# Performance work log

Hardware: AMD Instinct MI355X
Metric: run time of the kernel (lower is better)

Reference implementation:

```python
import jax, jax.numpy as jnp
import numpy as np

NUM_LAYERS = 4
EPS = 1e-8


def setup_inputs() -> dict:
    key = jax.random.key(0)
    ks = jax.random.split(key, 7)
    N, D, H = 8192, 1024, 4096
    return {
        "x": jax.random.normal(ks[0], (N, D), jnp.float32),
        "fc1_W": jax.random.normal(ks[1], (H, D), jnp.float32) * 0.02,
        "fc1_b": jax.random.normal(ks[2], (H,), jnp.float32) * 0.02,
        "fc2_W": jax.random.normal(ks[3], (D, H), jnp.float32) * 0.02,
        "fc2_b": jax.random.normal(ks[4], (D,), jnp.float32) * 0.02,
        "comp_W": jax.random.normal(ks[5], (NUM_LAYERS + 1, D, D), jnp.float32) * 0.03,
        "comp_b": jax.random.normal(ks[6], (NUM_LAYERS + 1, D), jnp.float32) * 0.03,
    }


def _block(x, fc1_W, fc1_b, fc2_W, fc2_b):
    # fc2(dropout(fc1(x))) in eval mode; relu is defined but never applied
    h = x @ fc1_W.T + fc1_b
    return h @ fc2_W.T + fc2_b


def _compute_loss(z, W, b):
    # out = Linear(z); per-row cosine_similarity(out_i.unsqueeze(1), out_i.unsqueeze(0))
    # reduces broadcast dim 1 -> vector c[j] = out[j]*sum(out) / max(|out[j]|*sqrt(y)*||out||, eps)
    # which torch broadcasts into constant rows of a [y,y] matrix; the
    # abs-diff accumulation over batch rows is then rank-1.
    out = z @ W.T + b                                # [N, y]
    y = out.shape[-1]
    S = out.sum(-1, keepdims=True)                   # [N, 1]
    n2 = jnp.sqrt((out * out).sum(-1, keepdims=True))  # [N, 1] row norms
    n1 = jnp.abs(out) * jnp.sqrt(jnp.asarray(y, out.dtype))  # [N, y]
    c = out * S / jnp.maximum(n1 * n2, EPS)          # [N, y]
    D = jnp.abs(c[1:] - c[:-1]).sum(0)               # [y]
    return jnp.broadcast_to(D, (y, y))               # [y, y]


def reference(x, fc1_W, fc1_b, fc2_W, fc2_b, comp_W, comp_b):
    inv = _block(x, fc1_W, fc1_b, fc2_W, fc2_b)
    loss = _compute_loss(inv, comp_W[0], comp_b[0])
    nxt = x - inv
    inv_total = inv
    for i in range(1, NUM_LAYERS + 1):
        inv_new = _block(nxt, fc1_W, fc1_b, fc2_W, fc2_b)
        inv_total = inv_total + inv_new
        loss = loss + _compute_loss(inv_new, comp_W[i], comp_b[i])
        nxt = nxt - inv_new
    return inv_total, nxt, loss
```

## Files before the change

kernel.cpp:

```cpp
#include <hip/hip_runtime.h>
#include <hip/hip_bf16.h>


#define NR 8192
#define DD 1024
#define HH 4096
#define NL 5
#define MSZ (DD * DD)

using bf16 = __hip_bfloat16;
typedef __attribute__((ext_vector_type(8))) short bf16x8;
typedef __attribute__((ext_vector_type(4))) float f32x4;
typedef _Float16 h4 __attribute__((ext_vector_type(4)));


__global__ void cvt_bf16_kernel(const float* __restrict__ in, bf16* __restrict__ out, int n4) {
  int i = blockIdx.x * 256 + threadIdx.x;
  int stride = gridDim.x * 256;
  union U { bf16 b[4]; uint2 u; };
  for (; i < n4; i += stride) {
    float4 v = ((const float4*)in)[i];
    U u;
    u.b[0] = __float2bfloat16(v.x); u.b[1] = __float2bfloat16(v.y);
    u.b[2] = __float2bfloat16(v.z); u.b[3] = __float2bfloat16(v.w);
    ((uint2*)out)[i] = u.u;
  }
}

__global__ void transpose_cvt_kernel(const float* __restrict__ in, bf16* __restrict__ out) {
  __shared__ bf16 tile[64][74];
  int c0 = blockIdx.x * 64;
  int r0 = blockIdx.y * 64;
  int col = threadIdx.x & 63;
  int row4 = threadIdx.x >> 6;
  #pragma unroll
  for (int j = 0; j < 16; ++j) {
    int r = row4 * 16 + j;
    tile[r][col] = __float2bfloat16(in[(size_t)(r0 + r) * DD + c0 + col]);
  }
  __syncthreads();
  #pragma unroll
  for (int j = 0; j < 16; ++j) {
    int r = row4 * 16 + j;
    out[(size_t)(c0 + r) * HH + r0 + col] = tile[col][r];
  }
}

__global__ void cvec_kernel(const float* __restrict__ fc1_b, const float* __restrict__ fc2_W,
                            const float* __restrict__ fc2_b, float* __restrict__ c) {
  int j = blockIdx.x;
  float s = 0.f;
  for (int k = threadIdx.x; k < HH; k += 256) s += fc1_b[k] * fc2_W[(size_t)j * HH + k];
  for (int o = 32; o; o >>= 1) s += __shfl_down(s, o);
  __shared__ float red[4];
  if ((threadIdx.x & 63) == 0) red[threadIdx.x >> 6] = s;
  __syncthreads();
  if (threadIdx.x == 0) c[j] = red[0] + red[1] + red[2] + red[3] + fc2_b[j];
}

__global__ void zero_kernel(float* __restrict__ p, int n) {
  int i = blockIdx.x * 256 + threadIdx.x;
  if (i < n) p[i] = 0.f;
}

__global__ void mbuild_kernel(const float* __restrict__ Cp,
                              bf16* __restrict__ M, bf16* __restrict__ Mt,
                              bf16* __restrict__ T, bf16* __restrict__ Tt) {
  __shared__ float tile[64][65];
  int n0 = blockIdx.x * 64, m0 = blockIdx.y * 64;
  int tn = threadIdx.x & 63, tm4 = threadIdx.x >> 6;
  #pragma unroll
  for (int j = 0; j < 16; ++j) {
    int m = tm4 * 16 + j;
    size_t idx = (size_t)(m0 + m) * DD + n0 + tn;
    float v = Cp[idx] + Cp[MSZ + idx] + Cp[2 * MSZ + idx] + Cp[3 * MSZ + idx];
    tile[m][tn] = v;
    float d = ((m0 + m) == (n0 + tn)) ? 1.f : 0.f;
    M[idx] = __float2bfloat16(v);
    T[idx] = __float2bfloat16(d - v);
  }
  __syncthreads();
  #pragma unroll
  for (int j = 0; j < 16; ++j) {
    int r = tm4 * 16 + j;
    float v = tile[tn][r];
    size_t idx = (size_t)(n0 + r) * DD + m0 + tn;
    float d = ((n0 + r) == (m0 + tn)) ? 1.f : 0.f;
    Mt[idx] = __float2bfloat16(v);
    Tt[idx] = __float2bfloat16(d - v);
  }
}

__global__ void sbuild_kernel(const bf16* __restrict__ Pw, bf16* __restrict__ S) {
  int idx = blockIdx.x * 256 + threadIdx.x;
  int m = idx >> 10, n = idx & (DD - 1);
  float v = (m == n) ? 1.f : 0.f;
  v += __bfloat162float(Pw[idx]) + __bfloat162float(Pw[MSZ + idx])
     + __bfloat162float(Pw[2 * MSZ + idx]) + __bfloat162float(Pw[3 * MSZ + idx]);
  S[idx] = __float2bfloat16(v);
}

__global__ void vecmat_kernel(const float* __restrict__ v, const bf16* __restrict__ Bt,
                              float* __restrict__ out) {
  int z = blockIdx.y, j = blockIdx.x;
  const bf16* row = Bt + (size_t)z * MSZ + (size_t)j * DD;
  float s = 0.f;
  for (int k = threadIdx.x; k < DD; k += 256) s += v[k] * __bfloat162float(row[k]);
  for (int o = 32; o; o >>= 1) s += __shfl_down(s, o);
  __shared__ float red[4];
  if ((threadIdx.x & 63) == 0) red[threadIdx.x >> 6] = s;
  __syncthreads();
  if (threadIdx.x == 0) out[(size_t)z * DD + j] = red[0] + red[1] + red[2] + red[3];
}

__global__ void biasall_kernel(const float* __restrict__ cvec, const float* __restrict__ ebuf,
                               const float* __restrict__ comp_W, const float* __restrict__ comp_b,
                               float* __restrict__ biasall) {
  int z = blockIdx.y, j = blockIdx.x;
  if (z == 0) {
    if (threadIdx.x == 0)
      biasall[j] = cvec[j] + ebuf[j] + ebuf[DD + j] + ebuf[2 * DD + j] + ebuf[3 * DD + j];
    return;
  }
  int i = z - 1;
  const float* e = (i == 0) ? cvec : ebuf + (size_t)(i - 1) * DD;
  const float* wr = comp_W + (size_t)i * MSZ + (size_t)j * DD;
  float s = 0.f;
  for (int k = threadIdx.x; k < DD; k += 256) s += e[k] * wr[k];
  for (int o = 32; o; o >>= 1) s += __shfl_down(s, o);
  __shared__ float red[4];
  if ((threadIdx.x & 63) == 0) red[threadIdx.x >> 6] = s;
  __syncthreads();
  if (threadIdx.x == 0)
    biasall[(size_t)z * DD + j] = red[0] + red[1] + red[2] + red[3] + comp_b[(size_t)i * DD + j];
}


__device__ __forceinline__ void async16(const bf16* g, bf16* l) {
  __builtin_amdgcn_global_load_lds(
      (const __attribute__((address_space(1))) void*)g,
      (__attribute__((address_space(3))) void*)l, 16, 0, 0);
}

__device__ __forceinline__ void gemm_core_async(
    const bf16* __restrict__ A, const bf16* __restrict__ B,
    int kBeg, int kEnd, int lda, int ldb, int bm, int bn,
    bf16* As, bf16* Bs, f32x4 acc[4][4])
{
  const int tid  = threadIdx.x;
  const int lane = tid & 63;
  const int wave = tid >> 6;
  const int wm = (wave & 1) * 64;
  const int wn = (wave >> 1) * 64;
  const int lr = lane >> 3;
  const int lcol = ((lane & 7) ^ lr) * 8;
  const bf16* gA = A + (size_t)(bm + wave * 32 + lr) * lda + lcol;
  const bf16* gB = B + (size_t)(bn + wave * 32 + lr) * ldb + lcol;
  bf16* lA = As + wave * 32 * 64;
  bf16* lB = Bs + wave * 32 * 64;

  for (int k0 = kBeg; k0 < kEnd; k0 += 64) {
    #pragma unroll
    for (int it = 0; it < 4; ++it) {
      async16(gA + (size_t)(it * 8) * lda + k0, lA + it * 8 * 64);
      async16(gB + (size_t)(it * 8) * ldb + k0, lB + it * 8 * 64);
    }
    __syncthreads();
    #pragma unroll
    for (int ks = 0; ks < 2; ++ks) {
      bf16x8 av[4], bv[4];
      #pragma unroll
      for (int i = 0; i < 4; ++i) {
        const int rr = i * 16 + (lane & 15);
        const int cc = ((ks * 4 + (lane >> 4)) ^ (lane & 7)) * 8;
        av[i] = *(const bf16x8*)(As + (wm + rr) * 64 + cc);
        bv[i] = *(const bf16x8*)(Bs + (wn + rr) * 64 + cc);
      }
      #pragma unroll
      for (int i = 0; i < 4; ++i)
        #pragma unroll
        for (int j = 0; j < 4; ++j)
          acc[i][j] = __builtin_amdgcn_mfma_f32_16x16x32_bf16(av[i], bv[j], acc[i][j], 0, 0, 0);
    }
    __syncthreads();
  }
}

#define GEMM_PROLOGUE \
  alignas(16) __shared__ bf16 As[128 * 64]; \
  alignas(16) __shared__ bf16 Bs[128 * 64]; \
  f32x4 acc[4][4] = {}; \
  const int lane = threadIdx.x & 63; \
  const int wm = ((threadIdx.x >> 6) & 1) * 64; \
  const int wn = ((threadIdx.x >> 6) >> 1) * 64;

__global__ __launch_bounds__(256, 2)
void gemm_splitk(const bf16* __restrict__ A, const bf16* __restrict__ B, float* __restrict__ Cp) {
  GEMM_PROLOGUE
  const int bm = blockIdx.y * 128, bn = blockIdx.x * 128;
  const int kb = blockIdx.z * (HH / 4);
  gemm_core_async(A, B, kb, kb + HH / 4, HH, HH, bm, bn, As, Bs, acc);
  float* C = Cp + (size_t)blockIdx.z * MSZ;
  #pragma unroll
  for (int i = 0; i < 4; ++i)
    #pragma unroll
    for (int j = 0; j < 4; ++j) {
      const int col = bn + wn + j * 16 + (lane & 15);
      #pragma unroll
      for (int r = 0; r < 4; ++r) {
        const int row = bm + wm + i * 16 + (lane >> 4) * 4 + r;
        C[(size_t)row * DD + col] = acc[i][j][r];
      }
    }
}

__global__ __launch_bounds__(256, 2)
void gemm_dual(const bf16* __restrict__ A, const bf16* __restrict__ B,
               bf16* __restrict__ Ct, bf16* __restrict__ Cn) {
  GEMM_PROLOGUE
  const int bm = blockIdx.y * 128, bn = blockIdx.x * 128;
  gemm_core_async(A, B, 0, DD, DD, DD, bm, bn, As, Bs, acc);
  #pragma unroll
  for (int i = 0; i < 4; ++i)
    #pragma unroll
    for (int j = 0; j < 4; ++j) {
      const int col = bn + wn + j * 16 + (lane & 15);
      const int row0 = bm + wm + i * 16 + (lane >> 4) * 4;
      union { bf16 b[4]; uint2 u; } pk;
      #pragma unroll
      for (int r = 0; r < 4; ++r) {
        bf16 v = __float2bfloat16(acc[i][j][r]);
        pk.b[r] = v;
        Cn[(size_t)(row0 + r) * DD + col] = v;
      }
      *(uint2*)(&Ct[(size_t)col * DD + row0]) = pk.u;
    }
}

__global__ __launch_bounds__(256, 2)
void gemm_b4(const bf16* __restrict__ A0, long astr, const bf16* __restrict__ B0, long bstr,
             bf16* __restrict__ C0, long cstr,
             const bf16* __restrict__ A2, const bf16* __restrict__ B2, bf16* __restrict__ C2,
             int zswitch) {
  GEMM_PROLOGUE
  const int z = blockIdx.z;
  const bf16* A; const bf16* B; bf16* C;
  if (z < zswitch) { A = A0 + (size_t)z * astr; B = B0 + (size_t)z * bstr; C = C0 + (size_t)z * cstr; }
  else             { A = A2; B = B2; C = C2; }
  const int bm = blockIdx.y * 128, bn = blockIdx.x * 128;
  gemm_core_async(A, B, 0, DD, DD, DD, bm, bn, As, Bs, acc);
  #pragma unroll
  for (int i = 0; i < 4; ++i)
    #pragma unroll
    for (int j = 0; j < 4; ++j) {
      const int col = bn + wn + j * 16 + (lane & 15);
      #pragma unroll
      for (int r = 0; r < 4; ++r) {
        const int row = bm + wm + i * 16 + (lane >> 4) * 4 + r;
        C[(size_t)row * DD + col] = __float2bfloat16(acc[i][j][r]);
      }
    }
}

__global__ __launch_bounds__(256, 2)
void gemm_main(const bf16* __restrict__ A, const bf16* __restrict__ Bb,
               const float* __restrict__ biasall, const float* __restrict__ x,
               float* __restrict__ invtot, float* __restrict__ nxtf,
               _Float16* __restrict__ out_h, float* __restrict__ Srow, float* __restrict__ Qrow) {
  GEMM_PROLOGUE
  const int bm = blockIdx.y * 128, bn = blockIdx.x * 128;
  gemm_core_async(A, Bb + (size_t)(bn >> 10) * MSZ, 0, DD, DD, DD, bm, bn & (DD - 1), As, Bs, acc);

  if (bn < DD) {
    #pragma unroll
    for (int i = 0; i < 4; ++i)
      #pragma unroll
      for (int j = 0; j < 4; ++j) {
        const int col = bn + wn + j * 16 + (lane & 15);
        const float bj = biasall[col];
        #pragma unroll
        for (int r = 0; r < 4; ++r) {
          const int row = bm + wm + i * 16 + (lane >> 4) * 4 + r;
          const float v = acc[i][j][r] + bj;
          const size_t idx = (size_t)row * DD + col;
          invtot[idx] = v;
          nxtf[idx] = x[idx] - v;
        }
      }
  } else {
    const int z = (bn >> 10) - 1;
    _Float16* oz = out_h + (size_t)z * NR * DD;
    const int cbase = bn & (DD - 1);
    float sv[4][4] = {}, qv[4][4] = {};
    #pragma unroll
    for (int i = 0; i < 4; ++i)
      #pragma unroll
      for (int j = 0; j < 4; ++j) {
        const int colg = bn + wn + j * 16 + (lane & 15);
        const int cj = cbase + wn + j * 16 + (lane & 15);
        const float bj = biasall[colg];
        #pragma unroll
        for (int r = 0; r < 4; ++r) {
          const int row = bm + wm + i * 16 + (lane >> 4) * 4 + r;
          const float v = acc[i][j][r] + bj;
          oz[(size_t)row * DD + cj] = (_Float16)v;
          sv[i][r] += v;
          qv[i][r] += v * v;
        }
      }
    #pragma unroll
    for (int i = 0; i < 4; ++i)
      #pragma unroll
      for (int r = 0; r < 4; ++r) {
        float s = sv[i][r], q = qv[i][r];
        #pragma unroll
        for (int off = 1; off < 16; off <<= 1) { s += __shfl_xor(s, off); q += __shfl_xor(q, off); }
        if ((lane & 15) == 0) {
          const int row = bm + wm + i * 16 + (lane >> 4) * 4 + r;
          atomicAdd(&Srow[(size_t)z * NR + row], s);
          atomicAdd(&Qrow[(size_t)z * NR + row], q);
        }
      }
  }
}


#define LCR 64
__global__ void losscol2_kernel(const _Float16* __restrict__ oh, const float* __restrict__ Srow,
                                const float* __restrict__ Qrow, float* __restrict__ Dtot) {
  const int z = blockIdx.y;
  const int n0 = blockIdx.x * LCR;
  int nend = n0 + LCR; if (nend > NR - 1) nend = NR - 1;
  const _Float16* base = oh + (size_t)z * NR * DD + (size_t)threadIdx.x * 4;
  const float* S = Srow + (size_t)z * NR;
  const float* Q = Qrow + (size_t)z * NR;
  float c[4], d[4] = {0.f, 0.f, 0.f, 0.f};
  auto compute = [&](int n, float* cv) {
    h4 o = *(const h4*)(base + (size_t)n * DD);
    float s = S[n];
    float t = 32.0f * sqrtf(Q[n]);
    #pragma unroll
    for (int k = 0; k < 4; ++k) {
      float ov = (float)o[k];
      cv[k] = ov * s / fmaxf(fabsf(ov) * t, 1e-8f);
    }
  };
  compute(n0, c);
  for (int n = n0 + 1; n <= nend; ++n) {
    float cn[4];
    compute(n, cn);
    #pragma unroll
    for (int k = 0; k < 4; ++k) { d[k] += fabsf(cn[k] - c[k]); c[k] = cn[k]; }
  }
  #pragma unroll
  for (int k = 0; k < 4; ++k) atomicAdd(&Dtot[z * DD + threadIdx.x * 4 + k], d[k]);
}

__global__ void writeloss_kernel(const float* __restrict__ Dtot, float* __restrict__ out) {
  int idx = blockIdx.x * 256 + threadIdx.x;
  int j = idx & (DD - 1);
  out[idx] = Dtot[j] + Dtot[DD + j] + Dtot[2 * DD + j] + Dtot[3 * DD + j] + Dtot[4 * DD + j];
}


extern "C" void kernel_launch(void* const* d_in, const int* in_sizes, int n_in,
                              void* d_out, int out_size, void* d_ws, size_t ws_size,
                              hipStream_t stream) {
  const float* x      = (const float*)d_in[0];
  const float* fc1_W  = (const float*)d_in[1];
  const float* fc1_b  = (const float*)d_in[2];
  const float* fc2_W  = (const float*)d_in[3];
  const float* fc2_b  = (const float*)d_in[4];
  const float* comp_W = (const float*)d_in[5];
  const float* comp_b = (const float*)d_in[6];

  float* invtot  = (float*)d_out;
  float* nxtf    = invtot + (size_t)NR * DD;
  float* lossout = invtot + (size_t)2 * NR * DD;

  char* w = (char*)d_ws;
  auto alloc = [&](size_t bytes) { char* p = w; w += (bytes + 255) & ~(size_t)255; return p; };
  bf16* x_bf     = (bf16*)alloc((size_t)NR * DD * 2);
  bf16* fc1T_bf  = (bf16*)alloc((size_t)DD * HH * 2);
  bf16* fc2_bf   = (bf16*)alloc((size_t)DD * HH * 2);
  bf16* compW_bf = (bf16*)alloc((size_t)NL * MSZ * 2);
  bf16* M_bf     = (bf16*)alloc((size_t)MSZ * 2);
  bf16* Mt_bf    = (bf16*)alloc((size_t)MSZ * 2);
  bf16* Tt_buf   = (bf16*)alloc((size_t)2 * MSZ * 2);
  bf16* Pw       = (bf16*)alloc((size_t)4 * MSZ * 2);
  bf16* S_bf     = (bf16*)alloc((size_t)MSZ * 2);
  bf16* Gt       = (bf16*)alloc((size_t)NL * MSZ * 2);
  bf16* Bbig     = (bf16*)alloc((size_t)6 * MSZ * 2);
  _Float16* out_h = (_Float16*)alloc((size_t)NL * NR * DD * 2);
  float* cvec    = (float*)alloc(DD * 4);
  float* ebuf    = (float*)alloc((size_t)4 * DD * 4);
  float* biasall = (float*)alloc((size_t)6 * DD * 4);
  float* stats   = (float*)alloc((size_t)(NL * DD + 2 * NL * NR) * 4);
  float* Dtot = stats;
  float* Srow = stats + NL * DD;
  float* Qrow = Srow + (size_t)NL * NR;
  float* Cp = (float*)out_h;
  (void)ws_size; (void)in_sizes; (void)n_in; (void)out_size;

  cvt_bf16_kernel<<<2048, 256, 0, stream>>>(x, x_bf, NR * DD / 4);
  cvt_bf16_kernel<<<1024, 256, 0, stream>>>(fc2_W, fc2_bf, DD * HH / 4);
  cvt_bf16_kernel<<<1024, 256, 0, stream>>>(comp_W, compW_bf, NL * MSZ / 4);
  transpose_cvt_kernel<<<dim3(DD / 64, HH / 64), 256, 0, stream>>>(fc1_W, fc1T_bf);
  cvec_kernel<<<DD, 256, 0, stream>>>(fc1_b, fc2_W, fc2_b, cvec);
  zero_kernel<<<(NL * DD + 2 * NL * NR + 255) / 256, 256, 0, stream>>>(stats, NL * DD + 2 * NL * NR);

  gemm_splitk<<<dim3(8, 8, 4), 256, 0, stream>>>(fc1T_bf, fc2_bf, Cp);
  mbuild_kernel<<<dim3(16, 16), 256, 0, stream>>>(Cp, M_bf, Mt_bf, Pw, Tt_buf);
  gemm_b4<<<dim3(8, 8, NL), 256, 0, stream>>>(compW_bf, MSZ, M_bf, 0, Gt, MSZ,
                                              nullptr, nullptr, nullptr, 99);
  hipMemcpyAsync(Bbig + MSZ, Gt, (size_t)MSZ * 2, hipMemcpyDeviceToDevice, stream);
  gemm_dual<<<dim3(8, 8), 256, 0, stream>>>(Pw, Tt_buf, Tt_buf + MSZ, Pw + MSZ);
  gemm_b4<<<dim3(8, 8, 2), 256, 0, stream>>>(Pw + MSZ, 0, Tt_buf, MSZ, Pw + 2 * MSZ, MSZ,
                                             nullptr, nullptr, nullptr, 99);
  sbuild_kernel<<<MSZ / 256, 256, 0, stream>>>(Pw, S_bf);
  gemm_b4<<<dim3(8, 8, NL), 256, 0, stream>>>(Gt + MSZ, MSZ, Pw, MSZ, Bbig + 2 * MSZ, MSZ,
                                              Mt_bf, S_bf, Bbig, 4);
  vecmat_kernel<<<dim3(DD, 2), 256, 0, stream>>>(cvec, Tt_buf, ebuf);
  vecmat_kernel<<<dim3(DD, 2), 256, 0, stream>>>(ebuf + DD, Tt_buf, ebuf + 2 * DD);
  biasall_kernel<<<dim3(DD, 6), 256, 0, stream>>>(cvec, ebuf, comp_W, comp_b, biasall);

  gemm_main<<<dim3(6 * DD / 128, NR / 128), 256, 0, stream>>>(
      x_bf, Bbig, biasall, x, invtot, nxtf, out_h, Srow, Qrow);

  losscol2_kernel<<<dim3(NR / LCR, NL), 256, 0, stream>>>(out_h, Srow, Qrow, Dtot);
  writeloss_kernel<<<MSZ / 256, 256, 0, stream>>>(Dtot, lossout);
}
```

Before: 527.8 us.

## Store only output sign bits for loss instead of fp16 outputs

The loss term c = out*S/max(|out|*sqrt(y)*||out||, eps) reduces to sign(out)*S/(32*||out||), so the GEMM epilogue now records one sign bit per element via wave ballots instead of writing the full fp16 projected outputs. A new loss kernel rebuilds c from the sign bits and the per-row sum and norm, computing abs-diffs per column from a shared-memory table of row scales. This removes about 80MB of fp16 writes and reads. The exact-zero/eps edge case is treated differently, and the bit-packed layout makes the loss kernel's access pattern scattered.

```diff
diff --git a/kernel.cpp b/kernel.cpp
--- a/kernel.cpp
+++ b/kernel.cpp
@@ -11,7 +11,6 @@
 using bf16 = __hip_bfloat16;
 typedef __attribute__((ext_vector_type(8))) short bf16x8;
 typedef __attribute__((ext_vector_type(4))) float f32x4;
-typedef _Float16 h4 __attribute__((ext_vector_type(4)));
 
 
 __global__ void cvt_bf16_kernel(const float* __restrict__ in, bf16* __restrict__ out, int n4) {
@@ -266,7 +265,8 @@
 void gemm_main(const bf16* __restrict__ A, const bf16* __restrict__ Bb,
                const float* __restrict__ biasall, const float* __restrict__ x,
                float* __restrict__ invtot, float* __restrict__ nxtf,
-               _Float16* __restrict__ out_h, float* __restrict__ Srow, float* __restrict__ Qrow) {
+               unsigned long long* __restrict__ sgn,
+               float* __restrict__ Srow, float* __restrict__ Qrow) {
   GEMM_PROLOGUE
   const int bm = blockIdx.y * 128, bn = blockIdx.x * 128;
   gemm_core_async(A, Bb + (size_t)(bn >> 10) * MSZ, 0, DD, DD, DD, bm, bn & (DD - 1), As, Bs, acc);
@@ -289,25 +289,28 @@
       }
   } else {
     const int z = (bn >> 10) - 1;
-    _Float16* oz = out_h + (size_t)z * NR * DD;
-    const int cbase = bn & (DD - 1);
+    const int rb = bm >> 7;
+    const int cb = (bn & (DD - 1)) >> 7;
+    const int wave = threadIdx.x >> 6;
+    unsigned long long keep = 0ULL;
     float sv[4][4] = {}, qv[4][4] = {};
     #pragma unroll
     for (int i = 0; i < 4; ++i)
       #pragma unroll
       for (int j = 0; j < 4; ++j) {
         const int colg = bn + wn + j * 16 + (lane & 15);
-        const int cj = cbase + wn + j * 16 + (lane & 15);
         const float bj = biasall[colg];
         #pragma unroll
         for (int r = 0; r < 4; ++r) {
-          const int row = bm + wm + i * 16 + (lane >> 4) * 4 + r;
           const float v = acc[i][j][r] + bj;
-          oz[(size_t)row * DD + cj] = (_Float16)v;
+          const unsigned long long bal = __ballot(v < 0.f);
+          if (lane == i * 16 + j * 4 + r) keep = bal;
           sv[i][r] += v;
           qv[i][r] += v * v;
         }
       }
+    const size_t wbase = ((((size_t)z * 64 + rb) * 8 + cb) * 4 + wave) * 64;
+    sgn[wbase + lane] = keep;
     #pragma unroll
     for (int i = 0; i < 4; ++i)
       #pragma unroll
@@ -325,35 +328,50 @@
 }
 
 
-#define LCR 64
-__global__ void losscol2_kernel(const _Float16* __restrict__ oh, const float* __restrict__ Srow,
-                                const float* __restrict__ Qrow, float* __restrict__ Dtot) {
+__global__ void losssign_kernel(const unsigned long long* __restrict__ sgn,
+                                const float* __restrict__ Srow, const float* __restrict__ Qrow,
+                                float* __restrict__ Dtot) {
   const int z = blockIdx.y;
-  const int n0 = blockIdx.x * LCR;
-  int nend = n0 + LCR; if (nend > NR - 1) nend = NR - 1;
-  const _Float16* base = oh + (size_t)z * NR * DD + (size_t)threadIdx.x * 4;
+  const int cg = blockIdx.x;
+  const int n0 = blockIdx.z * 1024;
+  __shared__ float rsh[1025];
   const float* S = Srow + (size_t)z * NR;
   const float* Q = Qrow + (size_t)z * NR;
-  float c[4], d[4] = {0.f, 0.f, 0.f, 0.f};
-  auto compute = [&](int n, float* cv) {
-    h4 o = *(const h4*)(base + (size_t)n * DD);
-    float s = S[n];
-    float t = 32.0f * sqrtf(Q[n]);
-    #pragma unroll
-    for (int k = 0; k < 4; ++k) {
-      float ov = (float)o[k];
-      cv[k] = ov * s / fmaxf(fabsf(ov) * t, 1e-8f);
-    }
+  for (int t = threadIdx.x; t < 1025; t += 256) {
+    int n = n0 + t; if (n > NR - 1) n = NR - 1;
+    rsh[t] = S[n] * rsqrtf(Q[n]) * 0.03125f;
+  }
+  __syncthreads();
+  const int c = threadIdx.x & 63;
+  const int q = threadIdx.x >> 6;
+  const int col = cg * 64 + c;
+  const int cb = col >> 7;
+  const int wsel = (col >> 6) & 1;
+  const int jf = (col >> 4) & 3;
+  const int c15 = col & 15;
+  const size_t zbase = (size_t)z * 64 * 8 * 4 * 64;
+  const int ns = n0 + q * 256;
+  int ne = ns + 256; if (ne > NR - 1) ne = NR - 1;
+
+  auto cval = [&](int n) -> float {
+    const int rbk = n >> 7, nl = n & 127;
+    const int wave = (nl >> 6) | (wsel << 1);
+    const int i = (nl >> 4) & 3, rg = (nl >> 2) & 3, r = nl & 3;
+    const size_t widx = zbase + ((((size_t)rbk * 8 + cb) * 4 + wave) * 64)
+                      + i * 16 + jf * 4 + r;
+    const unsigned long long wv = sgn[widx];
+    const float rv = rsh[n - n0];
+    return ((wv >> (rg * 16 + c15)) & 1ULL) ? -rv : rv;
   };
-  compute(n0, c);
-  for (int n = n0 + 1; n <= nend; ++n) {
-    float cn[4];
-    compute(n, cn);
-    #pragma unroll
-    for (int k = 0; k < 4; ++k) { d[k] += fabsf(cn[k] - c[k]); c[k] = cn[k]; }
-  }
-  #pragma unroll
-  for (int k = 0; k < 4; ++k) atomicAdd(&Dtot[z * DD + threadIdx.x * 4 + k], d[k]);
+
+  float d = 0.f;
+  float cprev = cval(ns);
+  for (int n = ns + 1; n <= ne; ++n) {
+    const float cn = cval(n);
+    d += fabsf(cn - cprev);
+    cprev = cn;
+  }
+  atomicAdd(&Dtot[z * DD + col], d);
 }
 
 __global__ void writeloss_kernel(const float* __restrict__ Dtot, float* __restrict__ out) {
@@ -391,7 +409,8 @@
   bf16* S_bf     = (bf16*)alloc((size_t)MSZ * 2);
   bf16* Gt       = (bf16*)alloc((size_t)NL * MSZ * 2);
   bf16* Bbig     = (bf16*)alloc((size_t)6 * MSZ * 2);
-  _Float16* out_h = (_Float16*)alloc((size_t)NL * NR * DD * 2);
+  unsigned long long* sgn = (unsigned long long*)alloc((size_t)NL * 64 * 8 * 4 * 64 * 8);
+  float* Cp      = (float*)alloc((size_t)4 * MSZ * 4);
   float* cvec    = (float*)alloc(DD * 4);
   float* ebuf    = (float*)alloc((size_t)4 * DD * 4);
   float* biasall = (float*)alloc((size_t)6 * DD * 4);
@@ -399,7 +418,6 @@
   float* Dtot = stats;
   float* Srow = stats + NL * DD;
   float* Qrow = Srow + (size_t)NL * NR;
-  float* Cp = (float*)out_h;
   (void)ws_size; (void)in_sizes; (void)n_in; (void)out_size;
 
   cvt_bf16_kernel<<<2048, 256, 0, stream>>>(x, x_bf, NR * DD / 4);
@@ -425,8 +443,8 @@
   biasall_kernel<<<dim3(DD, 6), 256, 0, stream>>>(cvec, ebuf, comp_W, comp_b, biasall);
 
   gemm_main<<<dim3(6 * DD / 128, NR / 128), 256, 0, stream>>>(
-      x_bf, Bbig, biasall, x, invtot, nxtf, out_h, Srow, Qrow);
-
-  losscol2_kernel<<<dim3(NR / LCR, NL), 256, 0, stream>>>(out_h, Srow, Qrow, Dtot);
+      x_bf, Bbig, biasall, x, invtot, nxtf, sgn, Srow, Qrow);
+
+  losssign_kernel<<<dim3(16, NL, 8), 256, 0, stream>>>(sgn, Srow, Qrow, Dtot);
   writeloss_kernel<<<MSZ / 256, 256, 0, stream>>>(Dtot, lossout);
 }
```

After: 513.2 us. 2.8% less time.
